# Optimization experiments

Measured on AMD Instinct MI355X. Metric: run time of the kernel, lower is better.

## Reference

```python
import jax, jax.numpy as jnp
import numpy as np

S, I, H, O = 4096, 64, 1024, 1


def setup_inputs() -> dict:
    key = jax.random.key(0)
    ks = jax.random.split(key, 8)
    k = 1.0 / np.sqrt(H)  # torch LSTM/Linear init scale
    u = lambda kk, shp: jax.random.uniform(kk, shp, jnp.float32, -k, k)
    return {
        "input_seq": jax.random.normal(ks[0], (S, I), jnp.float32),
        "W_ih": u(ks[1], (4 * H, I)),
        "W_hh": u(ks[2], (4 * H, H)),
        "b_ih": u(ks[3], (4 * H,)),
        "b_hh": u(ks[4], (4 * H,)),
        "W_lin": u(ks[5], (O, H)),
        "b_lin": u(ks[6], (O,)),
    }


def reference(input_seq, W_ih, W_hh, b_ih, b_hh, W_lin, b_lin):
    # Precompute input contributions to all gates in one GEMM: [S, 4H]
    x_gates = input_seq @ W_ih.T + (b_ih + b_hh)

    def step(carry, xg):
        h, c = carry
        g = xg + h @ W_hh.T  # [4H], gate order i, f, g, o (torch convention)
        i, f, gg, o = jnp.split(g, 4)
        i = jax.nn.sigmoid(i)
        f = jax.nn.sigmoid(f)
        gg = jnp.tanh(gg)
        o = jax.nn.sigmoid(o)
        c = f * c + i * gg
        h = o * jnp.tanh(c)
        return (h, c), None

    h0 = jnp.zeros((H,), x_gates.dtype)
    c0 = jnp.zeros((H,), x_gates.dtype)
    (h_last, _), _ = jax.lax.scan(step, (h0, c0), x_gates)
    # original applies linear to every step then takes [-1]; equivalent to
    # projecting only the last hidden state
    return h_last @ W_lin.T + b_lin  # [O]
```

## Files before the change

kernel.cpp:

```cpp
#include <hip/hip_runtime.h>


#define SEQ_LEN 4096
#define HID 1024
#define NBLK 128
#define TPB 512
#define HPB 8

__device__ __forceinline__ float fast_sigmoid(float x) {
    return __builtin_amdgcn_rcpf(1.0f + __builtin_amdgcn_exp2f(-1.4426950408889634f * x));
}
__device__ __forceinline__ float fast_tanh(float x) {
    return fmaf(-2.0f, __builtin_amdgcn_rcpf(1.0f + __builtin_amdgcn_exp2f(2.8853900817779268f * x)), 1.0f);
}

__global__ void lstm_init_kernel(unsigned long long* ws) {
    int t = threadIdx.x;
    #pragma unroll
    for (int k = 0; k < 8; ++k) ws[t + 256 * k] = 0ull;
}

__global__ __launch_bounds__(TPB, 1) void lstm_persistent_kernel(
    const float* __restrict__ input,
    const float* __restrict__ W_ih,
    const float* __restrict__ W_hh,
    const float* __restrict__ b_ih,
    const float* __restrict__ b_hh,
    const float* __restrict__ W_lin,
    const float* __restrict__ b_lin,
    float* __restrict__ out,
    unsigned long long* __restrict__ ws)
{
    const int t   = threadIdx.x;
    const int b   = blockIdx.x;
    const int w   = t >> 6;
    const int l   = t & 63;
    const int grp = l >> 4;
    const int sl  = l & 15;
    const int j   = HPB * b + w;
    const int row = grp * HID + j;

    unsigned long long* slot0 = ws;
    unsigned long long* slot1 = ws + HID;

    __shared__ float4 wlds4[17 * TPB];
    __shared__ float  hs[2][HID];
    __shared__ unsigned long long pub[HPB];
    __shared__ float  red[HPB];

    {
        const float4* Whh4 = (const float4*)(W_hh + (size_t)row * HID);
        #pragma unroll
        for (int c = 0; c < 16; ++c)
            wlds4[c * TPB + t] = Whh4[sl + 16 * c];
        wlds4[16 * TPB + t] = ((const float4*)(W_ih + (size_t)row * 64))[sl];
    }
    float bias[4];
    #pragma unroll
    for (int q = 0; q < 4; ++q) bias[q] = b_ih[q * HID + j] + b_hh[q * HID + j];
    if (t < HPB) pub[t] = 0ull;
    __syncthreads();

    const float4 W0  = wlds4[ 0 * TPB + t];
    const float4 W1  = wlds4[ 1 * TPB + t];
    const float4 W2  = wlds4[ 2 * TPB + t];
    const float4 W3  = wlds4[ 3 * TPB + t];
    const float4 W4  = wlds4[ 4 * TPB + t];
    const float4 W5  = wlds4[ 5 * TPB + t];
    const float4 W6  = wlds4[ 6 * TPB + t];
    const float4 W7  = wlds4[ 7 * TPB + t];
    const float4 W8  = wlds4[ 8 * TPB + t];
    const float4 W9  = wlds4[ 9 * TPB + t];
    const float4 W10 = wlds4[10 * TPB + t];
    const float4 W11 = wlds4[11 * TPB + t];
    const float4 W12 = wlds4[12 * TPB + t];
    const float4 W13 = wlds4[13 * TPB + t];
    const float4 W14 = wlds4[14 * TPB + t];
    const float4 W15 = wlds4[15 * TPB + t];
    const float4 W16 = wlds4[16 * TPB + t];

    const float4* xin4 = (const float4*)input;
    float c_state = 0.0f;

    for (int s = 0; s < SEQ_LEN; ++s) {
        float4 x4 = xin4[s * 16 + sl];

        unsigned long long* rs = (s & 1) ? slot1 : slot0;
        const unsigned tag = (unsigned)s;
        unsigned long long v0, v1;
        bool r0 = false, r1 = false;
        do {
            if (!r0) { v0 = __hip_atomic_load(&rs[t      ], __ATOMIC_RELAXED, __HIP_MEMORY_SCOPE_AGENT);
                       r0 = ((unsigned)(v0 >> 32) == tag); }
            if (!r1) { v1 = __hip_atomic_load(&rs[t + 512], __ATOMIC_RELAXED, __HIP_MEMORY_SCOPE_AGENT);
                       r1 = ((unsigned)(v1 >> 32) == tag); }
        } while (!(r0 && r1));

        float* hsb = hs[s & 1];
        hsb[t      ] = __uint_as_float((unsigned)(v0 & 0xffffffffull));
        hsb[t + 512] = __uint_as_float((unsigned)(v1 & 0xffffffffull));

        __syncthreads();

        const float4* hs4 = (const float4*)hsb;
        float a0 = 0.f, a1 = 0.f, a2 = 0.f, a3 = 0.f;
        #define FMA_CHUNK(Wc, c, acc) { float4 h4_ = hs4[16 * (c) + sl];      \
            acc = fmaf((Wc).x, h4_.x, acc); acc = fmaf((Wc).y, h4_.y, acc);   \
            acc = fmaf((Wc).z, h4_.z, acc); acc = fmaf((Wc).w, h4_.w, acc); }
        FMA_CHUNK(W0,  0, a0) FMA_CHUNK(W1,  1, a1)
        FMA_CHUNK(W2,  2, a2) FMA_CHUNK(W3,  3, a3)
        FMA_CHUNK(W4,  4, a0) FMA_CHUNK(W5,  5, a1)
        FMA_CHUNK(W6,  6, a2) FMA_CHUNK(W7,  7, a3)
        FMA_CHUNK(W8,  8, a0) FMA_CHUNK(W9,  9, a1)
        FMA_CHUNK(W10, 10, a2) FMA_CHUNK(W11, 11, a3)
        FMA_CHUNK(W12, 12, a0) FMA_CHUNK(W13, 13, a1)
        FMA_CHUNK(W14, 14, a2) FMA_CHUNK(W15, 15, a3)
        #undef FMA_CHUNK
        a0 = fmaf(W16.x, x4.x, a0); a1 = fmaf(W16.y, x4.y, a1);
        a2 = fmaf(W16.z, x4.z, a2); a3 = fmaf(W16.w, x4.w, a3);
        float acc = (a0 + a1) + (a2 + a3);

        acc += __shfl_xor(acc, 1);
        acc += __shfl_xor(acc, 2);
        acc += __shfl_xor(acc, 4);
        acc += __shfl_xor(acc, 8);

        float gi = __shfl(acc, 0)  + bias[0];
        float gf = __shfl(acc, 16) + bias[1];
        float gg = __shfl(acc, 32) + bias[2];
        float go = __shfl(acc, 48) + bias[3];

        float ig = fast_sigmoid(gi);
        float fg = fast_sigmoid(gf);
        float cg = fast_tanh(gg);
        float og = fast_sigmoid(go);
        c_state  = fmaf(fg, c_state, ig * cg);
        float hn = og * fast_tanh(c_state);

        const unsigned ntag = (unsigned)(s + 1);
        if (l == 0) {
            unsigned long long pv = ((unsigned long long)ntag << 32) |
                                    (unsigned long long)__float_as_uint(hn);
            __hip_atomic_store(&pub[w], pv, __ATOMIC_RELAXED, __HIP_MEMORY_SCOPE_WORKGROUP);
        }
        if (w == 0 && l < HPB) {
            unsigned long long pv;
            do {
                pv = __hip_atomic_load(&pub[l], __ATOMIC_RELAXED, __HIP_MEMORY_SCOPE_WORKGROUP);
            } while ((unsigned)(pv >> 32) != ntag);
            unsigned long long* wsl = (s & 1) ? slot0 : slot1;
            __hip_atomic_store(&wsl[HPB * b + l], pv, __ATOMIC_RELAXED, __HIP_MEMORY_SCOPE_AGENT);
        }
    }

    if (b == 0) {
        const unsigned tag = (unsigned)SEQ_LEN;
        unsigned long long v0, v1;
        bool r0 = false, r1 = false;
        do {
            if (!r0) { v0 = __hip_atomic_load(&slot0[t      ], __ATOMIC_RELAXED, __HIP_MEMORY_SCOPE_AGENT);
                       r0 = ((unsigned)(v0 >> 32) == tag); }
            if (!r1) { v1 = __hip_atomic_load(&slot0[t + 512], __ATOMIC_RELAXED, __HIP_MEMORY_SCOPE_AGENT);
                       r1 = ((unsigned)(v1 >> 32) == tag); }
        } while (!(r0 && r1));
        float p = __uint_as_float((unsigned)(v0 & 0xffffffffull)) * W_lin[t] +
                  __uint_as_float((unsigned)(v1 & 0xffffffffull)) * W_lin[t + 512];
        #pragma unroll
        for (int m = 32; m >= 1; m >>= 1) p += __shfl_xor(p, m);
        if (l == 0) red[w] = p;
        __syncthreads();
        if (t == 0) {
            float r = 0.f;
            #pragma unroll
            for (int k = 0; k < HPB; ++k) r += red[k];
            out[0] = r + b_lin[0];
        }
    }
}

extern "C" void kernel_launch(void* const* d_in, const int* in_sizes, int n_in,
                              void* d_out, int out_size, void* d_ws, size_t ws_size,
                              hipStream_t stream) {
    const float* input = (const float*)d_in[0];
    const float* W_ih  = (const float*)d_in[1];
    const float* W_hh  = (const float*)d_in[2];
    const float* b_ih  = (const float*)d_in[3];
    const float* b_hh  = (const float*)d_in[4];
    const float* W_lin = (const float*)d_in[5];
    const float* b_lin = (const float*)d_in[6];
    float* out = (float*)d_out;
    unsigned long long* ws = (unsigned long long*)d_ws;

    hipLaunchKernelGGL(lstm_init_kernel, dim3(1), dim3(256), 0, stream, ws);

    void* args[] = { (void*)&input, (void*)&W_ih, (void*)&W_hh, (void*)&b_ih,
                     (void*)&b_hh, (void*)&W_lin, (void*)&b_lin, (void*)&out, (void*)&ws };
    (void)hipLaunchCooperativeKernel((void*)lstm_persistent_kernel, dim3(NBLK), dim3(TPB),
                                     args, 0, stream);
}
```

Before: 8.035 ms.

## Replicate hidden-state mailbox per block pair to spread polling traffic

```diff
diff --git a/kernel.cpp b/kernel.cpp
--- a/kernel.cpp
+++ b/kernel.cpp
@@ -14,10 +14,10 @@
     return fmaf(-2.0f, __builtin_amdgcn_rcpf(1.0f + __builtin_amdgcn_exp2f(2.8853900817779268f * x)), 1.0f);
 }
 
-__global__ void lstm_init_kernel(unsigned long long* ws) {
-    int t = threadIdx.x;
-    #pragma unroll
-    for (int k = 0; k < 8; ++k) ws[t + 256 * k] = 0ull;
+__global__ void lstm_init_kernel(unsigned long long* ws, int n) {
+    int i = blockIdx.x * blockDim.x + threadIdx.x;
+    int stride = gridDim.x * blockDim.x;
+    for (; i < n; i += stride) ws[i] = 0ull;
 }
 
 __global__ __launch_bounds__(TPB, 1) void lstm_persistent_kernel(
@@ -29,7 +29,8 @@
     const float* __restrict__ W_lin,
     const float* __restrict__ b_lin,
     float* __restrict__ out,
-    unsigned long long* __restrict__ ws)
+    unsigned long long* __restrict__ ws,
+    int cshift)
 {
     const int t   = threadIdx.x;
     const int b   = blockIdx.x;
@@ -40,8 +41,8 @@
     const int j   = HPB * b + w;
     const int row = grp * HID + j;
 
-    unsigned long long* slot0 = ws;
-    unsigned long long* slot1 = ws + HID;
+    const int ncopies = NBLK >> cshift;
+    unsigned long long* mybox = ws + ((size_t)(b >> cshift) << 11);
 
     __shared__ float4 wlds4[17 * TPB];
     __shared__ float  hs[2][HID];
@@ -85,7 +86,7 @@
     for (int s = 0; s < SEQ_LEN; ++s) {
         float4 x4 = xin4[s * 16 + sl];
 
-        unsigned long long* rs = (s & 1) ? slot1 : slot0;
+        unsigned long long* rs = mybox + ((s & 1) << 10);
         const unsigned tag = (unsigned)s;
         unsigned long long v0, v1;
         bool r0 = false, r1 = false;
@@ -143,13 +144,17 @@
                                     (unsigned long long)__float_as_uint(hn);
             __hip_atomic_store(&pub[w], pv, __ATOMIC_RELAXED, __HIP_MEMORY_SCOPE_WORKGROUP);
         }
-        if (w == 0 && l < HPB) {
+        {
+            const int k = t & 7;
             unsigned long long pv;
             do {
-                pv = __hip_atomic_load(&pub[l], __ATOMIC_RELAXED, __HIP_MEMORY_SCOPE_WORKGROUP);
+                pv = __hip_atomic_load(&pub[k], __ATOMIC_RELAXED, __HIP_MEMORY_SCOPE_WORKGROUP);
             } while ((unsigned)(pv >> 32) != ntag);
-            unsigned long long* wsl = (s & 1) ? slot0 : slot1;
-            __hip_atomic_store(&wsl[HPB * b + l], pv, __ATOMIC_RELAXED, __HIP_MEMORY_SCOPE_AGENT);
+            const size_t boff = (size_t)(((s + 1) & 1) << 10) + (size_t)(HPB * b + k);
+            for (int c = t >> 3; c < ncopies; c += TPB / HPB) {
+                __hip_atomic_store(&ws[((size_t)c << 11) + boff], pv,
+                                   __ATOMIC_RELAXED, __HIP_MEMORY_SCOPE_AGENT);
+            }
         }
     }
 
@@ -158,9 +163,9 @@
         unsigned long long v0, v1;
         bool r0 = false, r1 = false;
         do {
-            if (!r0) { v0 = __hip_atomic_load(&slot0[t      ], __ATOMIC_RELAXED, __HIP_MEMORY_SCOPE_AGENT);
+            if (!r0) { v0 = __hip_atomic_load(&ws[t      ], __ATOMIC_RELAXED, __HIP_MEMORY_SCOPE_AGENT);
                        r0 = ((unsigned)(v0 >> 32) == tag); }
-            if (!r1) { v1 = __hip_atomic_load(&slot0[t + 512], __ATOMIC_RELAXED, __HIP_MEMORY_SCOPE_AGENT);
+            if (!r1) { v1 = __hip_atomic_load(&ws[t + 512], __ATOMIC_RELAXED, __HIP_MEMORY_SCOPE_AGENT);
                        r1 = ((unsigned)(v1 >> 32) == tag); }
         } while (!(r0 && r1));
         float p = __uint_as_float((unsigned)(v0 & 0xffffffffull)) * W_lin[t] +
@@ -191,10 +196,17 @@
     float* out = (float*)d_out;
     unsigned long long* ws = (unsigned long long*)d_ws;
 
-    hipLaunchKernelGGL(lstm_init_kernel, dim3(1), dim3(256), 0, stream, ws);
+    int cshift;
+    if      (ws_size >= (size_t)(NBLK >> 1) * 2048 * 8) cshift = 1;
+    else if (ws_size >= (size_t)(NBLK >> 4) * 2048 * 8) cshift = 4;
+    else                                                 cshift = 7;
+    int nzero = (NBLK >> cshift) * 2048;
+
+    hipLaunchKernelGGL(lstm_init_kernel, dim3(64), dim3(256), 0, stream, ws, nzero);
 
     void* args[] = { (void*)&input, (void*)&W_ih, (void*)&W_hh, (void*)&b_ih,
-                     (void*)&b_hh, (void*)&W_lin, (void*)&b_lin, (void*)&out, (void*)&ws };
+                     (void*)&b_hh, (void*)&W_lin, (void*)&b_lin, (void*)&out,
+                     (void*)&ws, (void*)&cshift };
     (void)hipLaunchCooperativeKernel((void*)lstm_persistent_kernel, dim3(NBLK), dim3(TPB),
                                      args, 0, stream);
 }
```

Result: slower. 9.493 ms (+18.1%).

## Replace block barrier with tagged LDS flags and per-wave direct publishing

Applied to the files above, without the earlier changes.

```diff
diff --git a/kernel.cpp b/kernel.cpp
--- a/kernel.cpp
+++ b/kernel.cpp
@@ -7,6 +7,11 @@
 #define TPB 512
 #define HPB 8
 
+#define ALD(p)    __hip_atomic_load((p), __ATOMIC_RELAXED, __HIP_MEMORY_SCOPE_AGENT)
+#define AST(p,v)  __hip_atomic_store((p), (v), __ATOMIC_RELAXED, __HIP_MEMORY_SCOPE_AGENT)
+#define LLD(p)    __hip_atomic_load((p), __ATOMIC_RELAXED, __HIP_MEMORY_SCOPE_WORKGROUP)
+#define LST(p,v)  __hip_atomic_store((p), (v), __ATOMIC_RELAXED, __HIP_MEMORY_SCOPE_WORKGROUP)
+
 __device__ __forceinline__ float fast_sigmoid(float x) {
     return __builtin_amdgcn_rcpf(1.0f + __builtin_amdgcn_exp2f(-1.4426950408889634f * x));
 }
@@ -15,9 +20,8 @@
 }
 
 __global__ void lstm_init_kernel(unsigned long long* ws) {
-    int t = threadIdx.x;
-    #pragma unroll
-    for (int k = 0; k < 8; ++k) ws[t + 256 * k] = 0ull;
+    int t = blockIdx.x * blockDim.x + threadIdx.x;
+    if (t < 2048) ws[t] = 0ull;
 }
 
 __global__ __launch_bounds__(TPB, 1) void lstm_persistent_kernel(
@@ -31,95 +35,105 @@
     float* __restrict__ out,
     unsigned long long* __restrict__ ws)
 {
-    const int t   = threadIdx.x;
-    const int b   = blockIdx.x;
-    const int w   = t >> 6;
-    const int l   = t & 63;
-    const int grp = l >> 4;
-    const int sl  = l & 15;
-    const int j   = HPB * b + w;
-    const int row = grp * HID + j;
-
-    unsigned long long* slot0 = ws;
-    unsigned long long* slot1 = ws + HID;
-
-    __shared__ float4 wlds4[17 * TPB];
-    __shared__ float  hs[2][HID];
-    __shared__ unsigned long long pub[HPB];
-    __shared__ float  red[HPB];
+    const int t = threadIdx.x;
+    const int b = blockIdx.x;
+    const int w = t >> 6;
+    const int l = t & 63;
+    const int j = HPB * b + w;
+
+    __shared__ float wlds[32 * 1024];
+    __shared__ float wih[32 * 64];
+    __shared__ unsigned long long hls[2 * HID];
+    __shared__ float red[HPB];
 
     {
-        const float4* Whh4 = (const float4*)(W_hh + (size_t)row * HID);
+        float4* wl4 = (float4*)wlds;
         #pragma unroll
-        for (int c = 0; c < 16; ++c)
-            wlds4[c * TPB + t] = Whh4[sl + 16 * c];
-        wlds4[16 * TPB + t] = ((const float4*)(W_ih + (size_t)row * 64))[sl];
+        for (int i = 0; i < 16; ++i) {
+            int flat = i * TPB + t;
+            int rr = flat >> 8;
+            int cc = flat & 255;
+            int row_g = ((rr >> 3) << 10) + HPB * b + (rr & 7);
+            wl4[flat] = ((const float4*)(W_hh + (size_t)row_g * HID))[cc];
+        }
+    }
+    {
+        float4* wi4 = (float4*)wih;
+        int rr = t >> 4, cc = t & 15;
+        int row_g = ((rr >> 3) << 10) + HPB * b + (rr & 7);
+        wi4[t] = ((const float4*)(W_ih + (size_t)row_g * 64))[cc];
     }
     float bias[4];
     #pragma unroll
-    for (int q = 0; q < 4; ++q) bias[q] = b_ih[q * HID + j] + b_hh[q * HID + j];
-    if (t < HPB) pub[t] = 0ull;
+    for (int q = 0; q < 4; ++q) bias[q] = b_ih[(q << 10) + j] + b_hh[(q << 10) + j];
+    #pragma unroll
+    for (int k = 0; k < 4; ++k) hls[t + TPB * k] = 0xFFFFFFFF00000000ull;
     __syncthreads();
 
-    const float4 W0  = wlds4[ 0 * TPB + t];
-    const float4 W1  = wlds4[ 1 * TPB + t];
-    const float4 W2  = wlds4[ 2 * TPB + t];
-    const float4 W3  = wlds4[ 3 * TPB + t];
-    const float4 W4  = wlds4[ 4 * TPB + t];
-    const float4 W5  = wlds4[ 5 * TPB + t];
-    const float4 W6  = wlds4[ 6 * TPB + t];
-    const float4 W7  = wlds4[ 7 * TPB + t];
-    const float4 W8  = wlds4[ 8 * TPB + t];
-    const float4 W9  = wlds4[ 9 * TPB + t];
-    const float4 W10 = wlds4[10 * TPB + t];
-    const float4 W11 = wlds4[11 * TPB + t];
-    const float4 W12 = wlds4[12 * TPB + t];
-    const float4 W13 = wlds4[13 * TPB + t];
-    const float4 W14 = wlds4[14 * TPB + t];
-    const float4 W15 = wlds4[15 * TPB + t];
-    const float4 W16 = wlds4[16 * TPB + t];
-
-    const float4* xin4 = (const float4*)input;
+#define DECLW(q) \
+    const float* wb##q = wlds + ((((q) << 3) | w) << 10) + l;                              \
+    const float W##q##_0 = wb##q[0],    W##q##_1 = wb##q[64],   W##q##_2 = wb##q[128],     \
+                W##q##_3 = wb##q[192],  W##q##_4 = wb##q[256],  W##q##_5 = wb##q[320],     \
+                W##q##_6 = wb##q[384],  W##q##_7 = wb##q[448],  W##q##_8 = wb##q[512],     \
+                W##q##_9 = wb##q[576],  W##q##_10 = wb##q[640], W##q##_11 = wb##q[704],    \
+                W##q##_12 = wb##q[768], W##q##_13 = wb##q[832], W##q##_14 = wb##q[896],    \
+                W##q##_15 = wb##q[960];
+    DECLW(0) DECLW(1) DECLW(2) DECLW(3)
+#undef DECLW
+    const float Wih0 = wih[((0 << 3) | w) * 64 + l];
+    const float Wih1 = wih[((1 << 3) | w) * 64 + l];
+    const float Wih2 = wih[((2 << 3) | w) * 64 + l];
+    const float Wih3 = wih[((3 << 3) | w) * 64 + l];
+
     float c_state = 0.0f;
 
     for (int s = 0; s < SEQ_LEN; ++s) {
-        float4 x4 = xin4[s * 16 + sl];
-
-        unsigned long long* rs = (s & 1) ? slot1 : slot0;
+        const int par = s & 1;
+        unsigned long long* rs = ws + (par << 10);
+        unsigned long long* hl = hls + (par << 10);
         const unsigned tag = (unsigned)s;
+
+        float xv = input[(s << 6) + l];
+
         unsigned long long v0, v1;
         bool r0 = false, r1 = false;
         do {
-            if (!r0) { v0 = __hip_atomic_load(&rs[t      ], __ATOMIC_RELAXED, __HIP_MEMORY_SCOPE_AGENT);
-                       r0 = ((unsigned)(v0 >> 32) == tag); }
-            if (!r1) { v1 = __hip_atomic_load(&rs[t + 512], __ATOMIC_RELAXED, __HIP_MEMORY_SCOPE_AGENT);
-                       r1 = ((unsigned)(v1 >> 32) == tag); }
+            if (!r0) { v0 = ALD(&rs[(w << 7) + l]);      r0 = ((unsigned)(v0 >> 32) == tag); }
+            if (!r1) { v1 = ALD(&rs[(w << 7) + 64 + l]); r1 = ((unsigned)(v1 >> 32) == tag); }
         } while (!(r0 && r1));
 
-        float* hsb = hs[s & 1];
-        hsb[t      ] = __uint_as_float((unsigned)(v0 & 0xffffffffull));
-        hsb[t + 512] = __uint_as_float((unsigned)(v1 & 0xffffffffull));
-
-        __syncthreads();
-
-        const float4* hs4 = (const float4*)hsb;
+        LST(&hl[(w << 7) + l],      v0);
+        LST(&hl[(w << 7) + 64 + l], v1);
+
+#define UINIT(c) unsigned long long u##c = LLD(&hl[((c) << 6) + l]);
+        UINIT(0)  UINIT(1)  UINIT(2)  UINIT(3)
+        UINIT(4)  UINIT(5)  UINIT(6)  UINIT(7)
+        UINIT(8)  UINIT(9)  UINIT(10) UINIT(11)
+        UINIT(12) UINIT(13) UINIT(14) UINIT(15)
+#undef UINIT
+
         float a0 = 0.f, a1 = 0.f, a2 = 0.f, a3 = 0.f;
-        #define FMA_CHUNK(Wc, c, acc) { float4 h4_ = hs4[16 * (c) + sl];      \
-            acc = fmaf((Wc).x, h4_.x, acc); acc = fmaf((Wc).y, h4_.y, acc);   \
-            acc = fmaf((Wc).z, h4_.z, acc); acc = fmaf((Wc).w, h4_.w, acc); }
-        FMA_CHUNK(W0,  0, a0) FMA_CHUNK(W1,  1, a1)
-        FMA_CHUNK(W2,  2, a2) FMA_CHUNK(W3,  3, a3)
-        FMA_CHUNK(W4,  4, a0) FMA_CHUNK(W5,  5, a1)
-        FMA_CHUNK(W6,  6, a2) FMA_CHUNK(W7,  7, a3)
-        FMA_CHUNK(W8,  8, a0) FMA_CHUNK(W9,  9, a1)
-        FMA_CHUNK(W10, 10, a2) FMA_CHUNK(W11, 11, a3)
-        FMA_CHUNK(W12, 12, a0) FMA_CHUNK(W13, 13, a1)
-        FMA_CHUNK(W14, 14, a2) FMA_CHUNK(W15, 15, a3)
-        #undef FMA_CHUNK
-        a0 = fmaf(W16.x, x4.x, a0); a1 = fmaf(W16.y, x4.y, a1);
-        a2 = fmaf(W16.z, x4.z, a2); a3 = fmaf(W16.w, x4.w, a3);
-        float acc = (a0 + a1) + (a2 + a3);
-
+#define CHUNK(c) {                                                                         \
+        while (!__all((int)((unsigned)(u##c >> 32) == tag)))                               \
+            u##c = LLD(&hl[((c) << 6) + l]);                                               \
+        const float hv = __uint_as_float((unsigned)(u##c & 0xffffffffull));                \
+        a0 = fmaf(W0_##c, hv, a0); a1 = fmaf(W1_##c, hv, a1);                              \
+        a2 = fmaf(W2_##c, hv, a2); a3 = fmaf(W3_##c, hv, a3); }
+        CHUNK(0)  CHUNK(1)  CHUNK(2)  CHUNK(3)
+        CHUNK(4)  CHUNK(5)  CHUNK(6)  CHUNK(7)
+        CHUNK(8)  CHUNK(9)  CHUNK(10) CHUNK(11)
+        CHUNK(12) CHUNK(13) CHUNK(14) CHUNK(15)
+#undef CHUNK
+        a0 = fmaf(Wih0, xv, a0); a1 = fmaf(Wih1, xv, a1);
+        a2 = fmaf(Wih2, xv, a2); a3 = fmaf(Wih3, xv, a3);
+
+        float x_, y_;
+        x_ = (l & 16) ? a0 : a1;  y_ = (l & 16) ? a1 : a0;
+        float s01 = y_ + __shfl_xor(x_, 16);
+        x_ = (l & 16) ? a2 : a3;  y_ = (l & 16) ? a3 : a2;
+        float s23 = y_ + __shfl_xor(x_, 16);
+        x_ = (l & 32) ? s01 : s23; y_ = (l & 32) ? s23 : s01;
+        float acc = y_ + __shfl_xor(x_, 32);
         acc += __shfl_xor(acc, 1);
         acc += __shfl_xor(acc, 2);
         acc += __shfl_xor(acc, 4);
@@ -137,19 +151,10 @@
         c_state  = fmaf(fg, c_state, ig * cg);
         float hn = og * fast_tanh(c_state);
 
-        const unsigned ntag = (unsigned)(s + 1);
         if (l == 0) {
-            unsigned long long pv = ((unsigned long long)ntag << 32) |
+            unsigned long long pv = ((unsigned long long)(unsigned)(s + 1) << 32) |
                                     (unsigned long long)__float_as_uint(hn);
-            __hip_atomic_store(&pub[w], pv, __ATOMIC_RELAXED, __HIP_MEMORY_SCOPE_WORKGROUP);
-        }
-        if (w == 0 && l < HPB) {
-            unsigned long long pv;
-            do {
-                pv = __hip_atomic_load(&pub[l], __ATOMIC_RELAXED, __HIP_MEMORY_SCOPE_WORKGROUP);
-            } while ((unsigned)(pv >> 32) != ntag);
-            unsigned long long* wsl = (s & 1) ? slot0 : slot1;
-            __hip_atomic_store(&wsl[HPB * b + l], pv, __ATOMIC_RELAXED, __HIP_MEMORY_SCOPE_AGENT);
+            AST(&ws[(((s + 1) & 1) << 10) + j], pv);
         }
     }
 
@@ -158,10 +163,8 @@
         unsigned long long v0, v1;
         bool r0 = false, r1 = false;
         do {
-            if (!r0) { v0 = __hip_atomic_load(&slot0[t      ], __ATOMIC_RELAXED, __HIP_MEMORY_SCOPE_AGENT);
-                       r0 = ((unsigned)(v0 >> 32) == tag); }
-            if (!r1) { v1 = __hip_atomic_load(&slot0[t + 512], __ATOMIC_RELAXED, __HIP_MEMORY_SCOPE_AGENT);
-                       r1 = ((unsigned)(v1 >> 32) == tag); }
+            if (!r0) { v0 = ALD(&ws[t      ]); r0 = ((unsigned)(v0 >> 32) == tag); }
+            if (!r1) { v1 = ALD(&ws[t + 512]); r1 = ((unsigned)(v1 >> 32) == tag); }
         } while (!(r0 && r1));
         float p = __uint_as_float((unsigned)(v0 & 0xffffffffull)) * W_lin[t] +
                   __uint_as_float((unsigned)(v1 & 0xffffffffull)) * W_lin[t + 512];
@@ -191,7 +194,7 @@
     float* out = (float*)d_out;
     unsigned long long* ws = (unsigned long long*)d_ws;
 
-    hipLaunchKernelGGL(lstm_init_kernel, dim3(1), dim3(256), 0, stream, ws);
+    hipLaunchKernelGGL(lstm_init_kernel, dim3(8), dim3(256), 0, stream, ws);
 
     void* args[] = { (void*)&input, (void*)&W_ih, (void*)&W_hh, (void*)&b_ih,
                      (void*)&b_hh, (void*)&W_lin, (void*)&b_lin, (void*)&out, (void*)&ws };
```

New measurement: 16.30 ms. 2.03x slower.

## Halve persistent blocks and compute two hidden units per warp

Applied to the files above, without the earlier changes.

```diff
diff --git a/kernel.cpp b/kernel.cpp
--- a/kernel.cpp
+++ b/kernel.cpp
@@ -3,9 +3,9 @@
 
 #define SEQ_LEN 4096
 #define HID 1024
-#define NBLK 128
+#define NBLK 64
 #define TPB 512
-#define HPB 8
+#define HPB 16
 
 __device__ __forceinline__ float fast_sigmoid(float x) {
     return __builtin_amdgcn_rcpf(1.0f + __builtin_amdgcn_exp2f(-1.4426950408889634f * x));
@@ -37,8 +37,10 @@
     const int l   = t & 63;
     const int grp = l >> 4;
     const int sl  = l & 15;
-    const int j   = HPB * b + w;
-    const int row = grp * HID + j;
+    const int j0  = HPB * b + w;
+    const int j1  = HPB * b + w + 8;
+    const int row0 = grp * HID + j0;
+    const int row1 = grp * HID + j1;
 
     unsigned long long* slot0 = ws;
     unsigned long long* slot1 = ws + HID;
@@ -46,18 +48,21 @@
     __shared__ float4 wlds4[17 * TPB];
     __shared__ float  hs[2][HID];
     __shared__ unsigned long long pub[HPB];
-    __shared__ float  red[HPB];
+    __shared__ float  red[8];
 
     {
-        const float4* Whh4 = (const float4*)(W_hh + (size_t)row * HID);
+        const float4* Whh4 = (const float4*)(W_hh + (size_t)row0 * HID);
         #pragma unroll
         for (int c = 0; c < 16; ++c)
             wlds4[c * TPB + t] = Whh4[sl + 16 * c];
-        wlds4[16 * TPB + t] = ((const float4*)(W_ih + (size_t)row * 64))[sl];
-    }
-    float bias[4];
+        wlds4[16 * TPB + t] = ((const float4*)(W_ih + (size_t)row0 * 64))[sl];
+    }
+    float bias0[4], bias1[4];
     #pragma unroll
-    for (int q = 0; q < 4; ++q) bias[q] = b_ih[q * HID + j] + b_hh[q * HID + j];
+    for (int q = 0; q < 4; ++q) {
+        bias0[q] = b_ih[q * HID + j0] + b_hh[q * HID + j0];
+        bias1[q] = b_ih[q * HID + j1] + b_hh[q * HID + j1];
+    }
     if (t < HPB) pub[t] = 0ull;
     __syncthreads();
 
@@ -78,9 +83,37 @@
     const float4 W14 = wlds4[14 * TPB + t];
     const float4 W15 = wlds4[15 * TPB + t];
     const float4 W16 = wlds4[16 * TPB + t];
+    __syncthreads();
+
+    {
+        const float4* Whh4 = (const float4*)(W_hh + (size_t)row1 * HID);
+        #pragma unroll
+        for (int c = 0; c < 16; ++c)
+            wlds4[c * TPB + t] = Whh4[sl + 16 * c];
+        wlds4[16 * TPB + t] = ((const float4*)(W_ih + (size_t)row1 * 64))[sl];
+    }
+    __syncthreads();
+
+    const float4 X0  = wlds4[ 0 * TPB + t];
+    const float4 X1  = wlds4[ 1 * TPB + t];
+    const float4 X2  = wlds4[ 2 * TPB + t];
+    const float4 X3  = wlds4[ 3 * TPB + t];
+    const float4 X4  = wlds4[ 4 * TPB + t];
+    const float4 X5  = wlds4[ 5 * TPB + t];
+    const float4 X6  = wlds4[ 6 * TPB + t];
+    const float4 X7  = wlds4[ 7 * TPB + t];
+    const float4 X8  = wlds4[ 8 * TPB + t];
+    const float4 X9  = wlds4[ 9 * TPB + t];
+    const float4 X10 = wlds4[10 * TPB + t];
+    const float4 X11 = wlds4[11 * TPB + t];
+    const float4 X12 = wlds4[12 * TPB + t];
+    const float4 X13 = wlds4[13 * TPB + t];
+    const float4 X14 = wlds4[14 * TPB + t];
+    const float4 X15 = wlds4[15 * TPB + t];
+    const float4 X16 = wlds4[16 * TPB + t];
 
     const float4* xin4 = (const float4*)input;
-    float c_state = 0.0f;
+    float c0_state = 0.0f, c1_state = 0.0f;
 
     for (int s = 0; s < SEQ_LEN; ++s) {
         float4 x4 = xin4[s * 16 + sl];
@@ -104,44 +137,59 @@
 
         const float4* hs4 = (const float4*)hsb;
         float a0 = 0.f, a1 = 0.f, a2 = 0.f, a3 = 0.f;
-        #define FMA_CHUNK(Wc, c, acc) { float4 h4_ = hs4[16 * (c) + sl];      \
-            acc = fmaf((Wc).x, h4_.x, acc); acc = fmaf((Wc).y, h4_.y, acc);   \
-            acc = fmaf((Wc).z, h4_.z, acc); acc = fmaf((Wc).w, h4_.w, acc); }
-        FMA_CHUNK(W0,  0, a0) FMA_CHUNK(W1,  1, a1)
-        FMA_CHUNK(W2,  2, a2) FMA_CHUNK(W3,  3, a3)
-        FMA_CHUNK(W4,  4, a0) FMA_CHUNK(W5,  5, a1)
-        FMA_CHUNK(W6,  6, a2) FMA_CHUNK(W7,  7, a3)
-        FMA_CHUNK(W8,  8, a0) FMA_CHUNK(W9,  9, a1)
-        FMA_CHUNK(W10, 10, a2) FMA_CHUNK(W11, 11, a3)
-        FMA_CHUNK(W12, 12, a0) FMA_CHUNK(W13, 13, a1)
-        FMA_CHUNK(W14, 14, a2) FMA_CHUNK(W15, 15, a3)
-        #undef FMA_CHUNK
+        float e0 = 0.f, e1 = 0.f, e2 = 0.f, e3 = 0.f;
+        #define FMA_CHUNK2(Wc, Xc, c, acc, ecc) { float4 h4_ = hs4[16 * (c) + sl]; \
+            acc = fmaf((Wc).x, h4_.x, acc); acc = fmaf((Wc).y, h4_.y, acc);        \
+            acc = fmaf((Wc).z, h4_.z, acc); acc = fmaf((Wc).w, h4_.w, acc);        \
+            ecc = fmaf((Xc).x, h4_.x, ecc); ecc = fmaf((Xc).y, h4_.y, ecc);        \
+            ecc = fmaf((Xc).z, h4_.z, ecc); ecc = fmaf((Xc).w, h4_.w, ecc); }
+        FMA_CHUNK2(W0,  X0,  0,  a0, e0) FMA_CHUNK2(W1,  X1,  1,  a1, e1)
+        FMA_CHUNK2(W2,  X2,  2,  a2, e2) FMA_CHUNK2(W3,  X3,  3,  a3, e3)
+        FMA_CHUNK2(W4,  X4,  4,  a0, e0) FMA_CHUNK2(W5,  X5,  5,  a1, e1)
+        FMA_CHUNK2(W6,  X6,  6,  a2, e2) FMA_CHUNK2(W7,  X7,  7,  a3, e3)
+        FMA_CHUNK2(W8,  X8,  8,  a0, e0) FMA_CHUNK2(W9,  X9,  9,  a1, e1)
+        FMA_CHUNK2(W10, X10, 10, a2, e2) FMA_CHUNK2(W11, X11, 11, a3, e3)
+        FMA_CHUNK2(W12, X12, 12, a0, e0) FMA_CHUNK2(W13, X13, 13, a1, e1)
+        FMA_CHUNK2(W14, X14, 14, a2, e2) FMA_CHUNK2(W15, X15, 15, a3, e3)
+        #undef FMA_CHUNK2
         a0 = fmaf(W16.x, x4.x, a0); a1 = fmaf(W16.y, x4.y, a1);
         a2 = fmaf(W16.z, x4.z, a2); a3 = fmaf(W16.w, x4.w, a3);
+        e0 = fmaf(X16.x, x4.x, e0); e1 = fmaf(X16.y, x4.y, e1);
+        e2 = fmaf(X16.z, x4.z, e2); e3 = fmaf(X16.w, x4.w, e3);
         float acc = (a0 + a1) + (a2 + a3);
-
-        acc += __shfl_xor(acc, 1);
-        acc += __shfl_xor(acc, 2);
-        acc += __shfl_xor(acc, 4);
-        acc += __shfl_xor(acc, 8);
-
-        float gi = __shfl(acc, 0)  + bias[0];
-        float gf = __shfl(acc, 16) + bias[1];
-        float gg = __shfl(acc, 32) + bias[2];
-        float go = __shfl(acc, 48) + bias[3];
-
-        float ig = fast_sigmoid(gi);
-        float fg = fast_sigmoid(gf);
-        float cg = fast_tanh(gg);
-        float og = fast_sigmoid(go);
-        c_state  = fmaf(fg, c_state, ig * cg);
-        float hn = og * fast_tanh(c_state);
+        float ecc = (e0 + e1) + (e2 + e3);
+
+        acc += __shfl_xor(acc, 1);  ecc += __shfl_xor(ecc, 1);
+        acc += __shfl_xor(acc, 2);  ecc += __shfl_xor(ecc, 2);
+        acc += __shfl_xor(acc, 4);  ecc += __shfl_xor(ecc, 4);
+        acc += __shfl_xor(acc, 8);  ecc += __shfl_xor(ecc, 8);
+
+        float gi0 = __shfl(acc, 0)  + bias0[0];
+        float gf0 = __shfl(acc, 16) + bias0[1];
+        float gg0 = __shfl(acc, 32) + bias0[2];
+        float go0 = __shfl(acc, 48) + bias0[3];
+        float gi1 = __shfl(ecc, 0)  + bias1[0];
+        float gf1 = __shfl(ecc, 16) + bias1[1];
+        float gg1 = __shfl(ecc, 32) + bias1[2];
+        float go1 = __shfl(ecc, 48) + bias1[3];
+
+        float ig0 = fast_sigmoid(gi0), ig1 = fast_sigmoid(gi1);
+        float fg0 = fast_sigmoid(gf0), fg1 = fast_sigmoid(gf1);
+        float cg0 = fast_tanh(gg0),    cg1 = fast_tanh(gg1);
+        float og0 = fast_sigmoid(go0), og1 = fast_sigmoid(go1);
+        c0_state = fmaf(fg0, c0_state, ig0 * cg0);
+        c1_state = fmaf(fg1, c1_state, ig1 * cg1);
+        float hn0 = og0 * fast_tanh(c0_state);
+        float hn1 = og1 * fast_tanh(c1_state);
 
         const unsigned ntag = (unsigned)(s + 1);
         if (l == 0) {
-            unsigned long long pv = ((unsigned long long)ntag << 32) |
-                                    (unsigned long long)__float_as_uint(hn);
-            __hip_atomic_store(&pub[w], pv, __ATOMIC_RELAXED, __HIP_MEMORY_SCOPE_WORKGROUP);
+            unsigned long long pv0 = ((unsigned long long)ntag << 32) |
+                                     (unsigned long long)__float_as_uint(hn0);
+            unsigned long long pv1 = ((unsigned long long)ntag << 32) |
+                                     (unsigned long long)__float_as_uint(hn1);
+            __hip_atomic_store(&pub[w],     pv0, __ATOMIC_RELAXED, __HIP_MEMORY_SCOPE_WORKGROUP);
+            __hip_atomic_store(&pub[w + 8], pv1, __ATOMIC_RELAXED, __HIP_MEMORY_SCOPE_WORKGROUP);
         }
         if (w == 0 && l < HPB) {
             unsigned long long pv;
@@ -172,7 +220,7 @@
         if (t == 0) {
             float r = 0.f;
             #pragma unroll
-            for (int k = 0; k < HPB; ++k) r += red[k];
+            for (int k = 0; k < 8; ++k) r += red[k];
             out[0] = r + b_lin[0];
         }
     }
```

Result: slower. 9.141 ms (+13.8%).
